# Kernel tuning notes

Measured on AMD Instinct MI355X. Metric: run time of the kernel, lower is better.

## Reference

```python
import jax, jax.numpy as jnp
import numpy as np

N = 1024
H = 1024
B, T = 64, 256


def setup_inputs() -> dict:
    key = jax.random.key(0)
    ks = jax.random.split(key, 12)
    inp = {
        "h_time": jax.random.normal(ks[0], (B, T, H), dtype=jnp.float32),
        "A_pearson": jax.random.uniform(ks[1], (N, N), dtype=jnp.float32),
        "E_dyn": jax.random.normal(ks[2], (N, H), dtype=jnp.float32) * 0.1,
        "alpha_raw": jnp.float32(0.5),
        "tau_raw": jnp.float32(1.0),
        # gate_gen: Linear(H, H//2) -> GELU -> Linear(H//2, N) -> Sigmoid
        "gate_W1": jax.random.normal(ks[3], (H, H // 2), dtype=jnp.float32) * (1.0 / np.sqrt(H)),
        "gate_b1": jnp.zeros((H // 2,), dtype=jnp.float32),
        "gate_W2": jax.random.normal(ks[4], (H // 2, N), dtype=jnp.float32) * (1.0 / np.sqrt(H // 2)),
        "gate_b2": jnp.zeros((N,), dtype=jnp.float32),
        "h2n_W": jax.random.normal(ks[5], (H, N), dtype=jnp.float32) * (1.0 / np.sqrt(H)),
        "h2n_b": jnp.zeros((N,), dtype=jnp.float32),
        "n2h_W": jax.random.normal(ks[6], (N, H), dtype=jnp.float32) * (1.0 / np.sqrt(N)),
        "n2h_b": jnp.zeros((H,), dtype=jnp.float32),
        "ln_w": jnp.ones((H,), dtype=jnp.float32),
        "ln_b": jnp.zeros((H,), dtype=jnp.float32),
    }
    return inp


def _layernorm(x, w, b, eps=1e-5):
    mu = x.mean(-1, keepdims=True)
    var = ((x - mu) ** 2).mean(-1, keepdims=True)
    return (x - mu) * jax.lax.rsqrt(var + eps) * w + b


def reference(h_time, A_pearson, E_dyn, alpha_raw, tau_raw,
              gate_W1, gate_b1, gate_W2, gate_b2,
              h2n_W, h2n_b, n2h_W, n2h_b, ln_w, ln_b):
    tau = jax.nn.softplus(tau_raw) + 1e-6
    alpha = jax.nn.sigmoid(alpha_raw)

    h_mean = h_time.mean(axis=(0, 1))                      # [H]
    E = E_dyn + h_mean[None, :]
    E_cur = E / jnp.maximum(jnp.linalg.norm(E, axis=-1, keepdims=True), 1e-12)  # F.normalize

    A_dyn = jax.nn.relu(E_cur @ E_cur.T)                   # [N,N]
    A_dyn = A_dyn / (A_dyn.sum(axis=-1, keepdims=True) + 1e-6)
    A_dyn = 0.5 * (A_dyn + A_dyn.T)
    A_base = alpha * A_pearson + (1.0 - alpha) * A_dyn

    h_gate = h_time.mean(axis=1)                           # [B,H]
    hid = jax.nn.gelu(h_gate @ gate_W1 + gate_b1, approximate=False)
    gamma = jax.nn.sigmoid(hid @ gate_W2 + gate_b2)        # [B,N]

    # Python loop over batch == row-scaling by mean gate
    A_mix = A_base * gamma.mean(axis=0)[:, None]           # [N,N]

    z_nodes = h_time @ h2n_W + h2n_b                       # [B,T,N]
    z_gcn = jnp.einsum('btn,mn->btm', z_nodes, A_mix)      # z_nodes @ A_mix.T
    msg_h = z_gcn @ n2h_W + n2h_b                          # [B,T,H]

    logits = (A_base @ E_cur) / tau                        # [N,H]
    node_attn = jax.nn.softmax(logits, axis=0)
    global_w = jnp.tanh(node_attn.mean(axis=0))            # [H]

    y = h_time * (1.0 + global_w) + msg_h
    return _layernorm(y, ln_w, ln_b)
```

## Files before the change

### kernel.cpp

```cpp
#include <hip/hip_runtime.h>
#include <math.h>

#define H 1024
#define Nn 1024
#define Bb 64
#define Tt 256
#define BT (Bb * Tt)

typedef unsigned short ushort_t;
typedef __attribute__((ext_vector_type(8))) short bf16x8;
typedef __attribute__((ext_vector_type(4))) float f32x4;


__device__ __forceinline__ ushort_t f2bf(float x) {
    union { float f; unsigned u; } v; v.f = x;
    unsigned r = v.u + 0x7FFFu + ((v.u >> 16) & 1u);
    return (ushort_t)(r >> 16);
}
__device__ __forceinline__ float bf2f(ushort_t h) {
    union { unsigned u; float f; } v; v.u = ((unsigned)h) << 16; return v.f;
}

__device__ __forceinline__ float block_reduce_sum_256(float v) {
    __shared__ float sbuf[4];
    __syncthreads();
    #pragma unroll
    for (int off = 32; off > 0; off >>= 1) v += __shfl_down(v, off, 64);
    int lane = threadIdx.x & 63, w = threadIdx.x >> 6;
    if (lane == 0) sbuf[w] = v;
    __syncthreads();
    if (threadIdx.x == 0) sbuf[0] = sbuf[0] + sbuf[1] + sbuf[2] + sbuf[3];
    __syncthreads();
    return sbuf[0];
}

__global__ void k_stage1(const float* __restrict__ h_time, float* __restrict__ hg_part,
                         ushort_t* __restrict__ ht_bf16, const float* __restrict__ n2h_b,
                         float* __restrict__ rowsumS, float* __restrict__ bias_h,
                         const float* __restrict__ n2h_W, const float* __restrict__ h2n_W,
                         const float* __restrict__ W1, const float* __restrict__ W2,
                         ushort_t* __restrict__ n2hWT_h, ushort_t* __restrict__ n2hWT_l,
                         ushort_t* __restrict__ h2nW_h, ushort_t* __restrict__ h2nW_l,
                         float* __restrict__ W1T, float* __restrict__ W2T) {
    __shared__ float tile[32][33];
    int id = blockIdx.x;
    if (id < 2048) {
        int b = id >> 5, r = id & 31;
        int z = r >> 2, cb = r & 3;
        int col = cb * 256 + threadIdx.x;
        if (b == 0 && z == 0) {
            rowsumS[col] = 0.f;
            bias_h[col] = n2h_b[col];
        }
        float s = 0.f;
        #pragma unroll 4
        for (int t = z * 32; t < z * 32 + 32; ++t) {
            size_t o = ((size_t)b * Tt + t) * H + col;
            float v = h_time[o];
            s += v;
            ht_bf16[o] = f2bf(v);
        }
        hg_part[(size_t)(b * 8 + z) * H + col] = s;
        return;
    }
    int tx = threadIdx.x & 31, ty = threadIdx.x >> 5;
    if (id < 3072) {
        int t = id - 2048;
        int i0 = (t >> 5) * 32, j0 = (t & 31) * 32;
        #pragma unroll
        for (int q = 0; q < 4; ++q)
            tile[ty + 8 * q][tx] = n2h_W[(size_t)(i0 + ty + 8 * q) * H + j0 + tx];
        __syncthreads();
        #pragma unroll
        for (int q = 0; q < 4; ++q) {
            float v = tile[tx][ty + 8 * q];
            size_t o = (size_t)(j0 + ty + 8 * q) * Nn + i0 + tx;
            ushort_t hh = f2bf(v);
            n2hWT_h[o] = hh;
            n2hWT_l[o] = f2bf(v - bf2f(hh));
        }
    } else if (id < 4096) {
        size_t idx = (size_t)(id - 3072) * 1024 + threadIdx.x * 4;
        float4 v = *(const float4*)&h2n_W[idx];
        float c[4] = {v.x, v.y, v.z, v.w};
        union { ushort_t u[4]; uint2 w; } ph, pl;
        #pragma unroll
        for (int q = 0; q < 4; ++q) {
            ph.u[q] = f2bf(c[q]);
            pl.u[q] = f2bf(c[q] - bf2f(ph.u[q]));
        }
        *(uint2*)&h2nW_h[idx] = ph.w;
        *(uint2*)&h2nW_l[idx] = pl.w;
    } else if (id < 4608) {
        int t = id - 4096;
        int i0 = (t >> 4) * 32, j0 = (t & 15) * 32;
        #pragma unroll
        for (int q = 0; q < 4; ++q)
            tile[ty + 8 * q][tx] = W1[(size_t)(i0 + ty + 8 * q) * 512 + j0 + tx];
        __syncthreads();
        #pragma unroll
        for (int q = 0; q < 4; ++q)
            W1T[(size_t)(j0 + ty + 8 * q) * 1024 + i0 + tx] = tile[tx][ty + 8 * q];
    } else {
        int t = id - 4608;
        int i0 = (t >> 5) * 32, j0 = (t & 31) * 32;
        #pragma unroll
        for (int q = 0; q < 4; ++q)
            tile[ty + 8 * q][tx] = W2[(size_t)(i0 + ty + 8 * q) * 1024 + j0 + tx];
        __syncthreads();
        #pragma unroll
        for (int q = 0; q < 4; ++q)
            W2T[(size_t)(j0 + ty + 8 * q) * 512 + i0 + tx] = tile[tx][ty + 8 * q];
    }
}

__global__ void k_stage2(const float* __restrict__ hg_part, float* __restrict__ h_gate,
                         float* __restrict__ h_mean) {
    int id = blockIdx.x;
    if (id < 256) {
        int b = id >> 2, cb = id & 3;
        int col = cb * 256 + threadIdx.x;
        float s = 0.f;
        #pragma unroll
        for (int z = 0; z < 8; ++z) s += hg_part[(size_t)(b * 8 + z) * H + col];
        h_gate[b * H + col] = s * (1.0f / Tt);
    } else {
        int h = (id - 256) * 256 + threadIdx.x;
        float s = 0.f;
        for (int r = 0; r < 512; ++r) s += hg_part[(size_t)r * H + h];
        h_mean[h] = s * (1.0f / (Bb * Tt));
    }
}

__global__ __launch_bounds__(256) void k_stage3(
    const float* __restrict__ E_dyn, const float* __restrict__ h_mean,
    ushort_t* __restrict__ E_b,
    const float* __restrict__ h_gate, const float* __restrict__ W1T,
    const float* __restrict__ b1, float* __restrict__ hid) {
    if (blockIdx.x < 1024) {
        int n = blockIdx.x;
        float e[4]; float ss = 0.f;
        #pragma unroll
        for (int q = 0; q < 4; ++q) {
            int h = threadIdx.x + 256 * q;
            e[q] = E_dyn[(size_t)n * H + h] + h_mean[h];
            ss += e[q] * e[q];
        }
        float tot = block_reduce_sum_256(ss);
        float scale = 1.0f / fmaxf(sqrtf(tot), 1e-12f);
        #pragma unroll
        for (int q = 0; q < 4; ++q) {
            int h = threadIdx.x + 256 * q;
            E_b[(size_t)n * H + h] = f2bf(e[q] * scale);
        }
        return;
    }
    int gid = (blockIdx.x - 1024) * 4 + (threadIdx.x >> 6);
    int lane = threadIdx.x & 63;
    int b = gid >> 9, j = gid & 511;
    const float* xr = h_gate + b * H;
    const float* wr = W1T + (size_t)j * H;
    float s = 0.f;
    #pragma unroll
    for (int it = 0; it < 4; ++it) {
        int k = it * 256 + lane * 4;
        float4 x4 = *(const float4*)&xr[k];
        float4 w4 = *(const float4*)&wr[k];
        s += x4.x * w4.x + x4.y * w4.y + x4.z * w4.z + x4.w * w4.w;
    }
    #pragma unroll
    for (int off = 32; off > 0; off >>= 1) s += __shfl_down(s, off, 64);
    if (lane == 0) {
        float a = s + b1[j];
        hid[b * 512 + j] = 0.5f * a * (1.0f + erff(a * 0.70710678118654752f));
    }
}

template <int PASSES, int EPI>
__device__ __forceinline__ void gemm64_body(
    int bx, int by,
    const ushort_t* __restrict__ Ah, const ushort_t* __restrict__ Al,
    const ushort_t* __restrict__ Bh, const ushort_t* __restrict__ Bl,
    ushort_t* __restrict__ O1, ushort_t* __restrict__ O2,
    float* __restrict__ fout, const float* __restrict__ fvec,
    int M, int N, int K) {
    constexpr int NST = (PASSES == 3) ? 4 : 2;
    __shared__ ushort_t sStage[NST * 64 * 64];
    ushort_t* sAh = sStage;
    ushort_t* sBh = sStage + 64 * 64;
    ushort_t* sAl = sStage + (NST == 4 ? 2 * 64 * 64 : 0);
    ushort_t* sBl = sStage + (NST == 4 ? 3 * 64 * 64 : 0);
    const int tid = threadIdx.x, wave = tid >> 6, lane = tid & 63;
    const int quad = lane >> 4, l16 = lane & 15;
    const int m0 = by * 64, n0 = bx * 64;
    const int wm = (wave >> 1) * 32, wn = (wave & 1) * 32;
    const int sw = (l16 & 7) << 3;

    f32x4 acc[2][2];
    #pragma unroll
    for (int i = 0; i < 2; ++i)
        #pragma unroll
        for (int j = 0; j < 2; ++j)
            acc[i][j] = (f32x4){0.f, 0.f, 0.f, 0.f};

    for (int k0 = 0; k0 < K; k0 += 64) {
        __syncthreads();
        #pragma unroll
        for (int inst = 0; inst < 2; ++inst) {
            const int cbase = (wave * 2 + inst) * 64;
            const int c = cbase + lane;
            const int row = c >> 3;
            const int q = (c & 7) ^ (row & 7);
            const size_t offA = (size_t)(m0 + row) * K + k0 + q * 8;
            const size_t offB = (size_t)(n0 + row) * K + k0 + q * 8;
            __builtin_amdgcn_global_load_lds(
                (const __attribute__((address_space(1))) unsigned int*)(Ah + offA),
                (__attribute__((address_space(3))) unsigned int*)&sAh[cbase * 8], 16, 0, 0);
            __builtin_amdgcn_global_load_lds(
                (const __attribute__((address_space(1))) unsigned int*)(Bh + offB),
                (__attribute__((address_space(3))) unsigned int*)&sBh[cbase * 8], 16, 0, 0);
            if constexpr (PASSES == 3) {
                __builtin_amdgcn_global_load_lds(
                    (const __attribute__((address_space(1))) unsigned int*)(Al + offA),
                    (__attribute__((address_space(3))) unsigned int*)&sAl[cbase * 8], 16, 0, 0);
                __builtin_amdgcn_global_load_lds(
                    (const __attribute__((address_space(1))) unsigned int*)(Bl + offB),
                    (__attribute__((address_space(3))) unsigned int*)&sBl[cbase * 8], 16, 0, 0);
            }
        }
        __syncthreads();
        #pragma unroll
        for (int half = 0; half < 2; ++half) {
            bf16x8 fah[2], fbh[2];
            bf16x8 fal[PASSES == 3 ? 2 : 1], fbl[PASSES == 3 ? 2 : 1];
            #pragma unroll
            for (int i = 0; i < 2; ++i) {
                const int ko = ((half * 4 + quad) << 3) ^ sw;
                fah[i] = *(const bf16x8*)&sAh[(wm + i * 16 + l16) * 64 + ko];
                fbh[i] = *(const bf16x8*)&sBh[(wn + i * 16 + l16) * 64 + ko];
                if constexpr (PASSES == 3) {
                    fal[i] = *(const bf16x8*)&sAl[(wm + i * 16 + l16) * 64 + ko];
                    fbl[i] = *(const bf16x8*)&sBl[(wn + i * 16 + l16) * 64 + ko];
                }
            }
            #pragma unroll
            for (int i = 0; i < 2; ++i)
                #pragma unroll
                for (int j = 0; j < 2; ++j) {
                    acc[i][j] = __builtin_amdgcn_mfma_f32_16x16x32_bf16(fah[i], fbh[j], acc[i][j], 0, 0, 0);
                    if constexpr (PASSES == 3) {
                        acc[i][j] = __builtin_amdgcn_mfma_f32_16x16x32_bf16(fah[i], fbl[j], acc[i][j], 0, 0, 0);
                        acc[i][j] = __builtin_amdgcn_mfma_f32_16x16x32_bf16(fal[i], fbh[j], acc[i][j], 0, 0, 0);
                    }
                }
        }
    }

    float fv[2];
    if constexpr (EPI == 2) {
        #pragma unroll
        for (int j = 0; j < 2; ++j) fv[j] = fvec[n0 + wn + j * 16 + l16];
    }
    #pragma unroll
    for (int i = 0; i < 2; ++i)
        #pragma unroll
        for (int r = 0; r < 4; ++r) {
            const int m = m0 + wm + i * 16 + quad * 4 + r;
            float rowacc = 0.f;
            #pragma unroll
            for (int j = 0; j < 2; ++j) {
                const size_t o = (size_t)m * N + n0 + wn + j * 16 + l16;
                float v = acc[i][j][r];
                if constexpr (EPI == 1) {
                    v = fmaxf(v, 0.f);
                    O1[o] = f2bf(v);
                    rowacc += v;
                } else if constexpr (EPI == 2) {
                    ushort_t hh = f2bf(v);
                    O1[o] = hh;
                    O2[o] = f2bf(v - bf2f(hh));
                    rowacc += v * fv[j];
                } else {
                    O1[o] = f2bf(v);
                }
            }
            if constexpr (EPI == 1 || EPI == 2) {
                rowacc += __shfl_xor(rowacc, 1);
                rowacc += __shfl_xor(rowacc, 2);
                rowacc += __shfl_xor(rowacc, 4);
                rowacc += __shfl_xor(rowacc, 8);
                if (l16 == 0) atomicAdd(&fout[m], rowacc);
            }
        }
}

__global__ __launch_bounds__(256) void k_stage4(
    const float* __restrict__ hid, const float* __restrict__ W2T,
    const float* __restrict__ b2, float* __restrict__ gmean,
    const ushort_t* __restrict__ E_b, ushort_t* __restrict__ Sb,
    float* __restrict__ rowsumS) {
    if (blockIdx.x < 256) {
        int n = blockIdx.x * 4 + (threadIdx.x >> 6);
        int lane = threadIdx.x & 63;
        const float* wr = W2T + (size_t)n * 512;
        float4 w0 = *(const float4*)&wr[lane * 4];
        float4 w1 = *(const float4*)&wr[256 + lane * 4];
        float bb = b2[n];
        float acc = 0.f;
        for (int b = 0; b < Bb; ++b) {
            const float* xr = hid + b * 512;
            float4 x0 = *(const float4*)&xr[lane * 4];
            float4 x1 = *(const float4*)&xr[256 + lane * 4];
            float s = x0.x * w0.x + x0.y * w0.y + x0.z * w0.z + x0.w * w0.w
                    + x1.x * w1.x + x1.y * w1.y + x1.z * w1.z + x1.w * w1.w;
            #pragma unroll
            for (int off = 32; off > 0; off >>= 1) s += __shfl_down(s, off, 64);
            if (lane == 0) acc += 1.0f / (1.0f + expf(-(s + bb)));
        }
        if (lane == 0) gmean[n] = acc * (1.0f / Bb);
        return;
    }
    int t = blockIdx.x - 256;
    gemm64_body<1, 1>(t & 15, t >> 4, E_b, nullptr, E_b, nullptr,
                      Sb, nullptr, rowsumS, nullptr, Nn, Nn, H);
}

__global__ void k_amixT(const ushort_t* __restrict__ Sb, const float* __restrict__ A_p,
                        const float* __restrict__ rowsumS, const float* __restrict__ gmean,
                        const float* __restrict__ alpha_raw,
                        ushort_t* __restrict__ Th, ushort_t* __restrict__ Tl) {
    __shared__ float tile[32][33];
    int i0 = blockIdx.y * 32, j0 = blockIdx.x * 32;
    int tx = threadIdx.x & 31, ty = threadIdx.x >> 5;
    float alpha = 1.0f / (1.0f + expf(-alpha_raw[0]));
    #pragma unroll
    for (int q = 0; q < 4; ++q) {
        int i = i0 + ty + 8 * q, j = j0 + tx;
        size_t idx = (size_t)i * Nn + j;
        float s = bf2f(Sb[idx]);
        float ad = 0.5f * s * (1.0f / (rowsumS[i] + 1e-6f) + 1.0f / (rowsumS[j] + 1e-6f));
        tile[ty + 8 * q][tx] = gmean[i] * fmaf(alpha, A_p[idx], (1.0f - alpha) * ad);
    }
    __syncthreads();
    #pragma unroll
    for (int q = 0; q < 4; ++q) {
        float v = tile[tx][ty + 8 * q];
        size_t o = (size_t)(j0 + ty + 8 * q) * Nn + i0 + tx;
        ushort_t hh = f2bf(v);
        Th[o] = hh;
        Tl[o] = f2bf(v - bf2f(hh));
    }
}

__global__ __launch_bounds__(256) void k_c1t(
    const ushort_t* __restrict__ Ah, const ushort_t* __restrict__ Al,
    const ushort_t* __restrict__ Bh, const ushort_t* __restrict__ Bl,
    ushort_t* __restrict__ O1, ushort_t* __restrict__ O2,
    float* __restrict__ fout, const float* __restrict__ fvec) {
    gemm64_body<3, 2>(blockIdx.x & 15, blockIdx.x >> 4, Ah, Al, Bh, Bl, O1, O2, fout, fvec,
                      Nn, Nn, Nn);
}
__global__ __launch_bounds__(256) void k_c2t(
    const ushort_t* __restrict__ Ah, const ushort_t* __restrict__ Al,
    const ushort_t* __restrict__ Bh, const ushort_t* __restrict__ Bl,
    ushort_t* __restrict__ O1) {
    gemm64_body<3, 3>(blockIdx.x & 15, blockIdx.x >> 4, Ah, Al, Bh, Bl, O1, nullptr,
                      nullptr, nullptr, Nn, Nn, Nn);
}

__global__ __launch_bounds__(256) void gemm_big(
    const ushort_t* __restrict__ A, const ushort_t* __restrict__ Bt,
    float* __restrict__ fout, const float* __restrict__ fvec,
    int M, int N, int K) {
    __shared__ ushort_t sStage[2 * 128 * 64];
    ushort_t* sAh = sStage;
    ushort_t* sBh = sStage + 128 * 64;

    const int tid = threadIdx.x;
    const int wave = tid >> 6, lane = tid & 63;
    const int quad = lane >> 4, l16 = lane & 15;
    int bx = blockIdx.x, g = bx & 7, s = bx >> 3;
    const int m0 = (g * 16 + (s >> 3)) * 128;
    const int n0 = (s & 7) * 128;
    const int wm = (wave >> 1) * 64, wn = (wave & 1) * 64;
    const int sw = (l16 & 7) << 3;

    f32x4 acc[4][4];
    #pragma unroll
    for (int i = 0; i < 4; ++i)
        #pragma unroll
        for (int j = 0; j < 4; ++j)
            acc[i][j] = (f32x4){0.f, 0.f, 0.f, 0.f};

    for (int k0 = 0; k0 < K; k0 += 64) {
        __syncthreads();
        #pragma unroll
        for (int inst = 0; inst < 4; ++inst) {
            const int cbase = (wave * 4 + inst) * 64;
            const int c = cbase + lane;
            const int row = c >> 3;
            const int q = (c & 7) ^ (row & 7);
            const size_t offA = (size_t)(m0 + row) * K + k0 + q * 8;
            const size_t offB = (size_t)(n0 + row) * K + k0 + q * 8;
            __builtin_amdgcn_global_load_lds(
                (const __attribute__((address_space(1))) unsigned int*)(A + offA),
                (__attribute__((address_space(3))) unsigned int*)&sAh[cbase * 8], 16, 0, 0);
            __builtin_amdgcn_global_load_lds(
                (const __attribute__((address_space(1))) unsigned int*)(Bt + offB),
                (__attribute__((address_space(3))) unsigned int*)&sBh[cbase * 8], 16, 0, 0);
        }
        __syncthreads();
        #pragma unroll
        for (int half = 0; half < 2; ++half) {
            bf16x8 fah[4], fbh[4];
            #pragma unroll
            for (int i = 0; i < 4; ++i) {
                const int ko = ((half * 4 + quad) << 3) ^ sw;
                fah[i] = *(const bf16x8*)&sAh[(wm + i * 16 + l16) * 64 + ko];
                fbh[i] = *(const bf16x8*)&sBh[(wn + i * 16 + l16) * 64 + ko];
            }
            #pragma unroll
            for (int i = 0; i < 4; ++i)
                #pragma unroll
                for (int j = 0; j < 4; ++j)
                    acc[i][j] = __builtin_amdgcn_mfma_f32_16x16x32_bf16(fah[i], fbh[j], acc[i][j], 0, 0, 0);
        }
    }
    __syncthreads();

    float* EsW = (float*)sStage + wave * (16 * 64);
    const float SC = 1.0009765622f;

    #pragma unroll
    for (int i = 0; i < 4; ++i) {
        #pragma unroll
        for (int j = 0; j < 4; ++j)
            #pragma unroll
            for (int r = 0; r < 4; ++r)
                EsW[(quad * 4 + r) * 64 + j * 16 + l16] = acc[i][j][r];
        __syncthreads();
        #pragma unroll
        for (int it = 0; it < 4; ++it) {
            const int idx = it * 64 + lane;
            const int row = idx >> 4, f4 = idx & 15;
            const int m = m0 + wm + i * 16 + row;
            const int coln = n0 + wn + f4 * 4;
            float4 v = *(const float4*)&EsW[row * 64 + f4 * 4];
            float4 b4 = *(const float4*)&fvec[coln];
            ushort4 h4 = *(const ushort4*)&A[(size_t)m * N + coln];
            float4 y;
            y.x = v.x + b4.x + SC * bf2f(h4.x);
            y.y = v.y + b4.y + SC * bf2f(h4.y);
            y.z = v.z + b4.z + SC * bf2f(h4.z);
            y.w = v.w + b4.w + SC * bf2f(h4.w);
            *(float4*)&fout[(size_t)m * N + coln] = y;
        }
        __syncthreads();
    }
}

__global__ __launch_bounds__(256) void k_final_ln(const float* __restrict__ ln_w,
                                                  const float* __restrict__ ln_b,
                                                  float* __restrict__ out) {
    int wave = threadIdx.x >> 6, lane = threadIdx.x & 63;
    size_t row = (size_t)blockIdx.x * 4 + wave;
    float4 v[4];
    float s = 0.f;
    #pragma unroll
    for (int q = 0; q < 4; ++q) {
        v[q] = *(const float4*)&out[row * H + q * 256 + lane * 4];
        s += v[q].x + v[q].y + v[q].z + v[q].w;
    }
    #pragma unroll
    for (int off = 1; off < 64; off <<= 1) s += __shfl_xor(s, off, 64);
    float mu = s * (1.0f / H);
    float ss = 0.f;
    #pragma unroll
    for (int q = 0; q < 4; ++q) {
        v[q].x -= mu; v[q].y -= mu; v[q].z -= mu; v[q].w -= mu;
        ss += v[q].x * v[q].x + v[q].y * v[q].y + v[q].z * v[q].z + v[q].w * v[q].w;
    }
    #pragma unroll
    for (int off = 1; off < 64; off <<= 1) ss += __shfl_xor(ss, off, 64);
    float rstd = rsqrtf(ss * (1.0f / H) + 1e-5f);
    #pragma unroll
    for (int q = 0; q < 4; ++q) {
        int k = q * 256 + lane * 4;
        float4 w4 = *(const float4*)&ln_w[k];
        float4 b4 = *(const float4*)&ln_b[k];
        float4 o;
        o.x = fmaf(v[q].x * rstd, w4.x, b4.x);
        o.y = fmaf(v[q].y * rstd, w4.y, b4.y);
        o.z = fmaf(v[q].z * rstd, w4.z, b4.z);
        o.w = fmaf(v[q].w * rstd, w4.w, b4.w);
        *(float4*)&out[row * H + k] = o;
    }
}


extern "C" void kernel_launch(void* const* d_in, const int* in_sizes, int n_in,
                              void* d_out, int out_size, void* d_ws, size_t ws_size,
                              hipStream_t stream) {
    const float* h_time    = (const float*)d_in[0];
    const float* A_p       = (const float*)d_in[1];
    const float* E_dyn     = (const float*)d_in[2];
    const float* alpha_raw = (const float*)d_in[3];
    const float* gW1   = (const float*)d_in[5];
    const float* gb1   = (const float*)d_in[6];
    const float* gW2   = (const float*)d_in[7];
    const float* gb2   = (const float*)d_in[8];
    const float* h2n_W = (const float*)d_in[9];
    const float* h2n_b = (const float*)d_in[10];
    const float* n2h_W = (const float*)d_in[11];
    const float* n2h_b = (const float*)d_in[12];
    const float* ln_w  = (const float*)d_in[13];
    const float* ln_b  = (const float*)d_in[14];
    float* out = (float*)d_out;

    float* ws = (float*)d_ws;
    float* h_gate  = ws;  ws += Bb * H;
    float* h_mean  = ws;  ws += H;
    float* rowsumS = ws;  ws += Nn;
    float* bias_h  = ws;  ws += H;
    float* hid     = ws;  ws += Bb * 512;
    float* gmean   = ws;  ws += Nn;
    float* W1T     = ws;  ws += 512 * H;
    float* W2T     = ws;  ws += H * 512;
    float* hg_part = ws;  ws += 512 * H;
    ws += 256;
    ushort_t* E_b     = (ushort_t*)ws;  ws += (Nn * H) / 2;
    ushort_t* Sb      = (ushort_t*)ws;  ws += (Nn * Nn) / 2;
    ushort_t* AmixT_h = (ushort_t*)ws;  ws += (Nn * Nn) / 2;
    ushort_t* AmixT_l = (ushort_t*)ws;  ws += (Nn * Nn) / 2;
    ushort_t* n2hWT_h = (ushort_t*)ws;  ws += (Nn * H) / 2;
    ushort_t* n2hWT_l = (ushort_t*)ws;  ws += (Nn * H) / 2;
    ushort_t* h2nW_h  = (ushort_t*)ws;  ws += (H * Nn) / 2;
    ushort_t* h2nW_l  = (ushort_t*)ws;  ws += (H * Nn) / 2;
    ushort_t* C1Th    = (ushort_t*)ws;  ws += (H * Nn) / 2;
    ushort_t* C1Tl    = (ushort_t*)ws;  ws += (H * Nn) / 2;
    ushort_t* C2t     = (ushort_t*)ws;  ws += (H * H) / 2;
    ushort_t* ht      = (ushort_t*)ws;  ws += ((size_t)BT * H) / 2;

    k_stage1<<<5120, 256, 0, stream>>>(h_time, hg_part, ht, n2h_b, rowsumS, bias_h,
                                       n2h_W, h2n_W, gW1, gW2,
                                       n2hWT_h, n2hWT_l, h2nW_h, h2nW_l, W1T, W2T);
    k_stage2<<<260, 256, 0, stream>>>(hg_part, h_gate, h_mean);
    k_stage3<<<9216, 256, 0, stream>>>(E_dyn, h_mean, E_b, h_gate, W1T, gb1, hid);
    k_stage4<<<512, 256, 0, stream>>>(hid, W2T, gb2, gmean, E_b, Sb, rowsumS);
    k_amixT<<<dim3(32, 32), 256, 0, stream>>>(Sb, A_p, rowsumS, gmean, alpha_raw, AmixT_h, AmixT_l);
    k_c1t<<<256, 256, 0, stream>>>(n2hWT_h, n2hWT_l, AmixT_h, AmixT_l, C1Th, C1Tl, bias_h, h2n_b);
    k_c2t<<<256, 256, 0, stream>>>(C1Th, C1Tl, h2nW_h, h2nW_l, C2t);
    gemm_big<<<1024, 256, 0, stream>>>(ht, C2t, out, bias_h, BT, H, H);
    k_final_ln<<<4096, 256, 0, stream>>>(ln_w, ln_b, out);
}
```

Measured before the change: 327.6 us.

## Double-buffer LDS staging in GEMM kernels to overlap loads with MFMA

Both the 64x64 GEMM body and the large 128x128 GEMM now use two LDS buffers. The next K tile is issued via global_load_lds while the current tile is computed, with one barrier per iteration instead of two. The big GEMM epilogue also writes all accumulators to LDS at once and drops the per-row-block barriers. This doubles LDS use (64KB for gemm_big and the 3-pass kernels), which may reduce occupancy. It also relies on the barrier after compute to make the async loads visible.

```diff
diff --git a/kernel.cpp b/kernel.cpp
--- a/kernel.cpp
+++ b/kernel.cpp
@@ -185,11 +185,8 @@
     float* __restrict__ fout, const float* __restrict__ fvec,
     int M, int N, int K) {
     constexpr int NST = (PASSES == 3) ? 4 : 2;
-    __shared__ ushort_t sStage[NST * 64 * 64];
-    ushort_t* sAh = sStage;
-    ushort_t* sBh = sStage + 64 * 64;
-    ushort_t* sAl = sStage + (NST == 4 ? 2 * 64 * 64 : 0);
-    ushort_t* sBl = sStage + (NST == 4 ? 3 * 64 * 64 : 0);
+    constexpr int BUFSZ = NST * 64 * 64;
+    __shared__ ushort_t sStage[2 * BUFSZ];
     const int tid = threadIdx.x, wave = tid >> 6, lane = tid & 63;
     const int quad = lane >> 4, l16 = lane & 15;
     const int m0 = by * 64, n0 = bx * 64;
@@ -203,8 +200,11 @@
         for (int j = 0; j < 2; ++j)
             acc[i][j] = (f32x4){0.f, 0.f, 0.f, 0.f};
 
-    for (int k0 = 0; k0 < K; k0 += 64) {
-        __syncthreads();
+    auto stage = [&](int buf, int k0) {
+        ushort_t* sAh = sStage + buf * BUFSZ;
+        ushort_t* sBh = sAh + 64 * 64;
+        ushort_t* sAl = sAh + 2 * 64 * 64;
+        ushort_t* sBl = sAh + 3 * 64 * 64;
         #pragma unroll
         for (int inst = 0; inst < 2; ++inst) {
             const int cbase = (wave * 2 + inst) * 64;
@@ -228,7 +228,13 @@
                     (__attribute__((address_space(3))) unsigned int*)&sBl[cbase * 8], 16, 0, 0);
             }
         }
-        __syncthreads();
+    };
+
+    auto compute = [&](int buf) {
+        const ushort_t* sAh = sStage + buf * BUFSZ;
+        const ushort_t* sBh = sAh + 64 * 64;
+        const ushort_t* sAl = sAh + 2 * 64 * 64;
+        const ushort_t* sBl = sAh + 3 * 64 * 64;
         #pragma unroll
         for (int half = 0; half < 2; ++half) {
             bf16x8 fah[2], fbh[2];
@@ -254,7 +260,18 @@
                     }
                 }
         }
-    }
+    };
+
+    stage(0, 0);
+    __syncthreads();
+    int cur = 0;
+    for (int k0 = 64; k0 < K; k0 += 64) {
+        stage(cur ^ 1, k0);
+        compute(cur);
+        __syncthreads();
+        cur ^= 1;
+    }
+    compute(cur);
 
     float fv[2];
     if constexpr (EPI == 2) {
@@ -372,9 +389,8 @@
     const ushort_t* __restrict__ A, const ushort_t* __restrict__ Bt,
     float* __restrict__ fout, const float* __restrict__ fvec,
     int M, int N, int K) {
-    __shared__ ushort_t sStage[2 * 128 * 64];
-    ushort_t* sAh = sStage;
-    ushort_t* sBh = sStage + 128 * 64;
+    constexpr int BUFSZ = 2 * 128 * 64;
+    __shared__ ushort_t sStage[2 * BUFSZ];
 
     const int tid = threadIdx.x;
     const int wave = tid >> 6, lane = tid & 63;
@@ -392,8 +408,9 @@
         for (int j = 0; j < 4; ++j)
             acc[i][j] = (f32x4){0.f, 0.f, 0.f, 0.f};
 
-    for (int k0 = 0; k0 < K; k0 += 64) {
-        __syncthreads();
+    auto stage = [&](int buf, int k0) {
+        ushort_t* sAh = sStage + buf * BUFSZ;
+        ushort_t* sBh = sAh + 128 * 64;
         #pragma unroll
         for (int inst = 0; inst < 4; ++inst) {
             const int cbase = (wave * 4 + inst) * 64;
@@ -409,7 +426,11 @@
                 (const __attribute__((address_space(1))) unsigned int*)(Bt + offB),
                 (__attribute__((address_space(3))) unsigned int*)&sBh[cbase * 8], 16, 0, 0);
         }
-        __syncthreads();
+    };
+
+    auto compute = [&](int buf) {
+        const ushort_t* sAh = sStage + buf * BUFSZ;
+        const ushort_t* sBh = sAh + 128 * 64;
         #pragma unroll
         for (int half = 0; half < 2; ++half) {
             bf16x8 fah[4], fbh[4];
@@ -425,27 +446,40 @@
                 for (int j = 0; j < 4; ++j)
                     acc[i][j] = __builtin_amdgcn_mfma_f32_16x16x32_bf16(fah[i], fbh[j], acc[i][j], 0, 0, 0);
         }
-    }
-    __syncthreads();
-
-    float* EsW = (float*)sStage + wave * (16 * 64);
+    };
+
+    stage(0, 0);
+    __syncthreads();
+    int cur = 0;
+    for (int k0 = 64; k0 < K; k0 += 64) {
+        stage(cur ^ 1, k0);
+        compute(cur);
+        __syncthreads();
+        cur ^= 1;
+    }
+    compute(cur);
+    __syncthreads();
+
+    float* EsW = (float*)sStage + wave * 4096;
     const float SC = 1.0009765622f;
 
     #pragma unroll
+    for (int i = 0; i < 4; ++i)
+        #pragma unroll
+        for (int j = 0; j < 4; ++j)
+            #pragma unroll
+            for (int r = 0; r < 4; ++r)
+                EsW[i * 1024 + (quad * 4 + r) * 64 + j * 16 + l16] = acc[i][j][r];
+    __syncthreads();
+    #pragma unroll
     for (int i = 0; i < 4; ++i) {
-        #pragma unroll
-        for (int j = 0; j < 4; ++j)
-            #pragma unroll
-            for (int r = 0; r < 4; ++r)
-                EsW[(quad * 4 + r) * 64 + j * 16 + l16] = acc[i][j][r];
-        __syncthreads();
         #pragma unroll
         for (int it = 0; it < 4; ++it) {
             const int idx = it * 64 + lane;
             const int row = idx >> 4, f4 = idx & 15;
             const int m = m0 + wm + i * 16 + row;
             const int coln = n0 + wn + f4 * 4;
-            float4 v = *(const float4*)&EsW[row * 64 + f4 * 4];
+            float4 v = *(const float4*)&EsW[i * 1024 + row * 64 + f4 * 4];
             float4 b4 = *(const float4*)&fvec[coln];
             ushort4 h4 = *(const ushort4*)&A[(size_t)m * N + coln];
             float4 y;
@@ -455,7 +489,6 @@
             y.w = v.w + b4.w + SC * bf2f(h4.w);
             *(float4*)&fout[(size_t)m * N + coln] = y;
         }
-        __syncthreads();
     }
 }
 
```

After: 316.6 us. -3.4%, faster.
